# Performance work log

Measured on AMD Instinct MI355X. Metric: run time of the kernel, lower is better.

## Reference

```python
import jax, jax.numpy as jnp
import numpy as np

L = 32            # fixed label space replacing torch.unique (labels in [0, L))
DELTA_AGG = 0.5
DELTA_DIS = 1.5
REG_W = 0.001


def safe_norm(sq):
    # sqrt with zero-safe gradient: returns 0 where sq == 0
    safe = jnp.where(sq > 0, sq, 1.0)
    return jnp.where(sq > 0, jnp.sqrt(safe), 0.0)


def _single(emb, instance, kernel, training_mask):
    D = emb.shape[0]
    tm = training_mask > 0.5
    kn = kernel > 0.5
    inst = jnp.where(tm, instance, 0).reshape(-1)          # (N,) masked instance labels
    inst_k = jnp.where(tm & kn, instance, 0).reshape(-1)   # (N,) kernel-region labels
    embf = emb.reshape(D, -1).T                            # (N, D)
    ones = jnp.ones(inst.shape, dtype=jnp.float32)

    # per-label kernel means (emb_mean), label 0 stays zero as in torch
    cnt_k = jax.ops.segment_sum(ones, inst_k, num_segments=L)            # (L,)
    sum_k = jax.ops.segment_sum(embf, inst_k, num_segments=L)            # (L, D)
    emb_mean = sum_k / jnp.maximum(cnt_k, 1.0)[:, None]
    emb_mean = emb_mean.at[0].set(0.0)

    present = cnt_k > 0
    num_instance = jnp.sum(present.astype(jnp.int32))
    nz = present & (jnp.arange(L) > 0)

    # aggregation loss: per-pixel distance to own instance's kernel mean
    diff = embf - emb_mean[inst]                                          # (N, D)
    dist = safe_norm(jnp.sum(diff * diff, axis=1))
    val = jnp.log(jax.nn.relu(dist - DELTA_AGG) ** 2 + 1.0)
    sum_v = jax.ops.segment_sum(val, inst, num_segments=L)
    cnt = jax.ops.segment_sum(ones, inst, num_segments=L)
    l_agg_per = sum_v / jnp.maximum(cnt, 1.0)
    l_agg = jnp.sum(jnp.where(nz, l_agg_per, 0.0)) / jnp.maximum(num_instance - 1, 1)

    # discrimination loss: all pairs of distinct non-background present labels
    pdiff = emb_mean[:, None, :] - emb_mean[None, :, :]                   # (L, L, D)
    pdist = safe_norm(jnp.sum(pdiff * pdiff, axis=-1))
    pval = jnp.log(jax.nn.relu(2.0 * DELTA_DIS - pdist) ** 2 + 1.0)
    pmask = nz[:, None] & nz[None, :] & ~jnp.eye(L, dtype=bool)
    n_pairs = jnp.sum(pmask.astype(jnp.float32))
    l_dis = jnp.sum(jnp.where(pmask, pval, 0.0)) / jnp.maximum(n_pairs, 1.0)
    l_dis = jnp.where(num_instance > 2, l_dis, 0.0)

    # regularizer over the num_instance present columns of emb_mean
    reg = jnp.log(safe_norm(jnp.sum(emb_mean * emb_mean, axis=1)) + 1.0)
    l_reg = jnp.sum(jnp.where(present, reg, 0.0)) / jnp.maximum(num_instance, 1) * REG_W

    loss = l_agg + l_dis + l_reg
    return jnp.where(num_instance <= 1, 0.0, loss)


def setup_inputs() -> dict:
    key = jax.random.key(0)
    k1, k2, k3, k4 = jax.random.split(key, 4)
    B, D, H, W = 8, 4, 736, 736
    emb = jax.random.normal(k1, (B, D, H, W), dtype=jnp.float32)
    instance = jax.random.randint(k2, (B, H, W), 0, L, dtype=jnp.int32)
    kernel = jax.random.uniform(k3, (B, H, W), dtype=jnp.float32)
    training_mask = jax.random.uniform(k4, (B, H, W), dtype=jnp.float32)
    return {"emb": emb, "instance": instance, "kernel": kernel, "training_mask": training_mask}


def reference(emb, instance, kernel, training_mask):
    return jax.vmap(_single)(emb, instance, kernel, training_mask)
```

## Files before the change

kernel.cpp:

```cpp
#include <hip/hip_runtime.h>

#define LBL 32
#define NPIX (736 * 736)
#define NQ (NPIX / 4)
#define QPB 512
#define NBA 265
#define BATCH 8
#define DELTA_AGG 0.5f
#define DELTA_DIS 1.5f
#define REG_W 0.001f

#define LAB_BASE 0
#define PA_BASE (BATCH * NQ)
#define RED_BASE (PA_BASE + BATCH * NBA * 160)
#define PC_BASE (RED_BASE + BATCH * 256)

__global__ __launch_bounds__(256) void kA(
    const float* __restrict__ emb, const int* __restrict__ inst,
    const float* __restrict__ kern, const float* __restrict__ mask,
    float* __restrict__ ws) {
  const int b = blockIdx.y;
  const int t = threadIdx.x;
  __shared__ float s_cnt[LBL];
  __shared__ float s_sum[LBL * 4];
  if (t < LBL) s_cnt[t] = 0.f;
  if (t < LBL * 4) s_sum[t] = 0.f;
  __syncthreads();

  const long base = (long)b * NPIX;
  const float* eb = emb + (long)b * 4 * NPIX;
  const int4* ip = (const int4*)(inst + base);
  const float4* kp = (const float4*)(kern + base);
  const float4* mp = (const float4*)(mask + base);
  const float4* p0 = (const float4*)(eb);
  const float4* p1 = (const float4*)(eb + NPIX);
  const float4* p2 = (const float4*)(eb + 2 * NPIX);
  const float4* p3 = (const float4*)(eb + 3 * NPIX);

  const int q0 = blockIdx.x * QPB + t;
  const int q1 = q0 + 256;
  const bool v1 = (q1 < NQ);

  const int4 iva = ip[q0];
  const float4 kva = kp[q0], mva = mp[q0];
  const float4 ea0 = p0[q0], ea1 = p1[q0], ea2 = p2[q0], ea3 = p3[q0];
  int4 ivb;
  float4 kvb, mvb, eb0, eb1, eb2, eb3;
  if (v1) {
    ivb = ip[q1]; kvb = kp[q1]; mvb = mp[q1];
    eb0 = p0[q1]; eb1 = p1[q1]; eb2 = p2[q1]; eb3 = p3[q1];
  }

  bool has0 = false;
  unsigned int* labp = (unsigned int*)(ws + LAB_BASE) + (size_t)b * NQ;

  {
    const int labs[4] = {iva.x, iva.y, iva.z, iva.w};
    const float ks[4] = {kva.x, kva.y, kva.z, kva.w};
    const float ms[4] = {mva.x, mva.y, mva.z, mva.w};
    const float c0[4] = {ea0.x, ea0.y, ea0.z, ea0.w};
    const float c1[4] = {ea1.x, ea1.y, ea1.z, ea1.w};
    const float c2[4] = {ea2.x, ea2.y, ea2.z, ea2.w};
    const float c3[4] = {ea3.x, ea3.y, ea3.z, ea3.w};
    unsigned int labw = 0;
#pragma unroll
    for (int j = 0; j < 4; j++) {
      const bool m = ms[j] > 0.5f;
      const int li = m ? labs[j] : 0;
      const int lk = (m && ks[j] > 0.5f) ? labs[j] : 0;
      labw |= ((unsigned int)li) << (8 * j);
      if (lk > 0) {
        atomicAdd(&s_cnt[lk], 1.0f);
        atomicAdd(&s_sum[lk * 4 + 0], c0[j]);
        atomicAdd(&s_sum[lk * 4 + 1], c1[j]);
        atomicAdd(&s_sum[lk * 4 + 2], c2[j]);
        atomicAdd(&s_sum[lk * 4 + 3], c3[j]);
      } else {
        has0 = true;
      }
    }
    labp[q0] = labw;
  }
  if (v1) {
    const int labs[4] = {ivb.x, ivb.y, ivb.z, ivb.w};
    const float ks[4] = {kvb.x, kvb.y, kvb.z, kvb.w};
    const float ms[4] = {mvb.x, mvb.y, mvb.z, mvb.w};
    const float c0[4] = {eb0.x, eb0.y, eb0.z, eb0.w};
    const float c1[4] = {eb1.x, eb1.y, eb1.z, eb1.w};
    const float c2[4] = {eb2.x, eb2.y, eb2.z, eb2.w};
    const float c3[4] = {eb3.x, eb3.y, eb3.z, eb3.w};
    unsigned int labw = 0;
#pragma unroll
    for (int j = 0; j < 4; j++) {
      const bool m = ms[j] > 0.5f;
      const int li = m ? labs[j] : 0;
      const int lk = (m && ks[j] > 0.5f) ? labs[j] : 0;
      labw |= ((unsigned int)li) << (8 * j);
      if (lk > 0) {
        atomicAdd(&s_cnt[lk], 1.0f);
        atomicAdd(&s_sum[lk * 4 + 0], c0[j]);
        atomicAdd(&s_sum[lk * 4 + 1], c1[j]);
        atomicAdd(&s_sum[lk * 4 + 2], c2[j]);
        atomicAdd(&s_sum[lk * 4 + 3], c3[j]);
      } else {
        has0 = true;
      }
    }
    labp[q1] = labw;
  }

  if (has0) s_cnt[0] = 1.0f;
  __syncthreads();
  float* po = ws + PA_BASE + ((size_t)b * NBA + blockIdx.x) * 160;
  if (t < 160) po[t] = (t < 32) ? s_cnt[t] : s_sum[t - 32];
}

__global__ __launch_bounds__(256) void kB(float* __restrict__ ws) {
  const int b = blockIdx.y;
  const int col = blockIdx.x * 4 + (threadIdx.x >> 6);
  const int lane = threadIdx.x & 63;
  const float* pa = ws + PA_BASE + (size_t)b * NBA * 160 + col;
  float s = 0.f;
  for (int g = lane; g < NBA; g += 64) s += pa[(size_t)g * 160];
#pragma unroll
  for (int o = 32; o > 0; o >>= 1) s += __shfl_down(s, o);
  if (lane == 0) ws[RED_BASE + b * 256 + col] = s;
}

__global__ __launch_bounds__(256) void kC(
    const float* __restrict__ emb, float* __restrict__ ws) {
  const int b = blockIdx.y;
  const int t = threadIdx.x;
  __shared__ float s_mean[LBL * 4];
  __shared__ float s_val[LBL];
  __shared__ float s_cta[LBL];
  const float* rd = ws + RED_BASE + b * 256;
  if (t < LBL * 4) {
    const int l = t >> 2;
    s_mean[t] = (l == 0) ? 0.f : rd[32 + t] / fmaxf(rd[l], 1.0f);
  }
  if (t < LBL) {
    s_val[t] = 0.f;
    s_cta[t] = 0.f;
  }
  __syncthreads();

  const float* ebase = emb + (long)b * 4 * NPIX;
  const float4* p0 = (const float4*)(ebase);
  const float4* p1 = (const float4*)(ebase + NPIX);
  const float4* p2 = (const float4*)(ebase + 2 * NPIX);
  const float4* p3 = (const float4*)(ebase + 3 * NPIX);
  const unsigned int* labp = (const unsigned int*)(ws + LAB_BASE) + (size_t)b * NQ;

  const int q0 = blockIdx.x * QPB + t;
  const int q1 = q0 + 256;
  const bool v1 = (q1 < NQ);

  const unsigned int lwa = labp[q0];
  const float4 ea0 = p0[q0], ea1 = p1[q0], ea2 = p2[q0], ea3 = p3[q0];
  unsigned int lwb = 0;
  float4 eb0, eb1, eb2, eb3;
  if (v1) {
    lwb = labp[q1];
    eb0 = p0[q1]; eb1 = p1[q1]; eb2 = p2[q1]; eb3 = p3[q1];
  }

  {
    const float c0[4] = {ea0.x, ea0.y, ea0.z, ea0.w};
    const float c1[4] = {ea1.x, ea1.y, ea1.z, ea1.w};
    const float c2[4] = {ea2.x, ea2.y, ea2.z, ea2.w};
    const float c3[4] = {ea3.x, ea3.y, ea3.z, ea3.w};
#pragma unroll
    for (int j = 0; j < 4; j++) {
      const int li = (lwa >> (8 * j)) & 0xFF;
      if (li > 0) {
        const float d0 = c0[j] - s_mean[li * 4 + 0];
        const float d1 = c1[j] - s_mean[li * 4 + 1];
        const float d2 = c2[j] - s_mean[li * 4 + 2];
        const float d3 = c3[j] - s_mean[li * 4 + 3];
        const float sq = d0 * d0 + d1 * d1 + d2 * d2 + d3 * d3;
        const float dist = (sq > 0.f) ? sqrtf(sq) : 0.f;
        const float tt = fmaxf(dist - DELTA_AGG, 0.f);
        atomicAdd(&s_val[li], logf(fmaf(tt, tt, 1.0f)));
        atomicAdd(&s_cta[li], 1.0f);
      }
    }
  }
  if (v1) {
    const float c0[4] = {eb0.x, eb0.y, eb0.z, eb0.w};
    const float c1[4] = {eb1.x, eb1.y, eb1.z, eb1.w};
    const float c2[4] = {eb2.x, eb2.y, eb2.z, eb2.w};
    const float c3[4] = {eb3.x, eb3.y, eb3.z, eb3.w};
#pragma unroll
    for (int j = 0; j < 4; j++) {
      const int li = (lwb >> (8 * j)) & 0xFF;
      if (li > 0) {
        const float d0 = c0[j] - s_mean[li * 4 + 0];
        const float d1 = c1[j] - s_mean[li * 4 + 1];
        const float d2 = c2[j] - s_mean[li * 4 + 2];
        const float d3 = c3[j] - s_mean[li * 4 + 3];
        const float sq = d0 * d0 + d1 * d1 + d2 * d2 + d3 * d3;
        const float dist = (sq > 0.f) ? sqrtf(sq) : 0.f;
        const float tt = fmaxf(dist - DELTA_AGG, 0.f);
        atomicAdd(&s_val[li], logf(fmaf(tt, tt, 1.0f)));
        atomicAdd(&s_cta[li], 1.0f);
      }
    }
  }
  __syncthreads();
  float* po = ws + PC_BASE + ((size_t)b * NBA + blockIdx.x) * 64;
  if (t < 64) po[t] = (t < 32) ? s_val[t] : s_cta[t - 32];
}

__global__ __launch_bounds__(1024) void kD(const float* __restrict__ ws,
                                           float* __restrict__ out) {
  const int b = blockIdx.x;
  const int t = threadIdx.x;
  const int col = t >> 4, sub = t & 15;
  const float* pc = ws + PC_BASE + (size_t)b * NBA * 64 + col;
  float s = 0.f;
  for (int g = sub; g < NBA; g += 16) s += pc[(size_t)g * 64];
  __shared__ float red[64][17];
  red[col][sub] = s;

  const float* rd = ws + RED_BASE + b * 256;
  __shared__ float sm[LBL * 4];
  __shared__ float scc[LBL];
  if (t >= 512 && t < 640) {
    const int e = t - 512, l = e >> 2;
    sm[e] = (l == 0) ? 0.f : rd[32 + e] / fmaxf(rd[l], 1.0f);
  } else if (t >= 640 && t < 672) {
    scc[t - 640] = rd[t - 640];
  }
  __syncthreads();
  __shared__ float svca[64];
  if (t < 64) {
    float v = 0.f;
#pragma unroll
    for (int k = 0; k < 16; k++) v += red[t][k];
    svca[t] = v;
  }
  __syncthreads();

  if (t < 64) {
    const int lane = t;
    const bool pres = (lane < LBL) && (scc[lane & 31] > 0.f);
    const unsigned long long bal_p = __ballot(pres);
    const int num_instance = __popcll(bal_p);
    const bool nz = pres && (lane > 0);
    const unsigned long long bal_nz = __ballot(nz);

    float agg = 0.f;
    if (nz) agg = svca[lane] / fmaxf(svca[32 + lane], 1.0f);

    float reg = 0.f;
    if (pres) {
      float sq = 0.f;
#pragma unroll
      for (int d = 0; d < 4; d++) sq += sm[lane * 4 + d] * sm[lane * 4 + d];
      const float nrm = (sq > 0.f) ? sqrtf(sq) : 0.f;
      reg = logf(nrm + 1.0f);
    }

    float dis = 0.f, npair = 0.f;
    for (int pi = lane; pi < LBL * LBL; pi += 64) {
      const int i = pi >> 5, j = pi & 31;
      if (i != j && ((bal_nz >> i) & 1ull) && ((bal_nz >> j) & 1ull)) {
        float sq = 0.f;
#pragma unroll
        for (int d = 0; d < 4; d++) {
          const float df = sm[i * 4 + d] - sm[j * 4 + d];
          sq += df * df;
        }
        const float pdist = (sq > 0.f) ? sqrtf(sq) : 0.f;
        const float tt = fmaxf(2.0f * DELTA_DIS - pdist, 0.f);
        dis += logf(fmaf(tt, tt, 1.0f));
        npair += 1.0f;
      }
    }

#pragma unroll
    for (int o = 32; o > 0; o >>= 1) {
      agg += __shfl_down(agg, o);
      reg += __shfl_down(reg, o);
      dis += __shfl_down(dis, o);
      npair += __shfl_down(npair, o);
    }

    if (lane == 0) {
      const float l_agg = agg / fmaxf((float)(num_instance - 1), 1.0f);
      const float l_dis = (num_instance > 2) ? dis / fmaxf(npair, 1.0f) : 0.f;
      const float l_reg = reg / fmaxf((float)num_instance, 1.0f) * REG_W;
      const float loss = l_agg + l_dis + l_reg;
      out[b] = (num_instance <= 1) ? 0.f : loss;
    }
  }
}

extern "C" void kernel_launch(void* const* d_in, const int* in_sizes, int n_in,
                              void* d_out, int out_size, void* d_ws,
                              size_t ws_size, hipStream_t stream) {
  const float* emb = (const float*)d_in[0];
  const int* instance = (const int*)d_in[1];
  const float* kern = (const float*)d_in[2];
  const float* mask = (const float*)d_in[3];
  float* out = (float*)d_out;
  float* ws = (float*)d_ws;

  dim3 gridA(NBA, BATCH);
  kA<<<gridA, 256, 0, stream>>>(emb, instance, kern, mask, ws);
  dim3 gridB(40, BATCH);
  kB<<<gridB, 256, 0, stream>>>(ws);
  kC<<<gridA, 256, 0, stream>>>(emb, ws);
  kD<<<BATCH, 1024, 0, stream>>>(ws, out);
}
```

Baseline: 196.1 us.

## Cache bf16 copy of embeddings in first pass, reuse in aggregation pass

The first pass now writes a packed bf16 copy of the four embedding channels per pixel into the workspace. It also counts the masked instance pixels there, so the aggregation kernel no longer reads the fp32 embeddings or does the count atomics. The aggregation kernel reads 8 bytes per pixel instead of 16, and the partial-sum layouts and the final reduction are adjusted to match. In exchange, the first pass writes extra data, and the per-pixel distances are computed from bf16-rounded embeddings, which reduces accuracy.

```diff
diff --git a/kernel.cpp b/kernel.cpp
--- a/kernel.cpp
+++ b/kernel.cpp
@@ -10,10 +10,23 @@
 #define DELTA_DIS 1.5f
 #define REG_W 0.001f
 
-#define LAB_BASE 0
-#define PA_BASE (BATCH * NQ)
-#define RED_BASE (PA_BASE + BATCH * NBA * 160)
+#define CE_BASE 0
+#define LAB_BASE (BATCH * NPIX * 2)
+#define PA_BASE (LAB_BASE + BATCH * NQ)
+#define RED_BASE (PA_BASE + BATCH * NBA * 192)
 #define PC_BASE (RED_BASE + BATCH * 256)
+
+__device__ __forceinline__ unsigned short f2bf(float f) {
+  unsigned int u = __float_as_uint(f);
+  unsigned int r = u + 0x7FFFu + ((u >> 16) & 1u);
+  return (unsigned short)(r >> 16);
+}
+__device__ __forceinline__ float bfl(unsigned int w) {
+  return __uint_as_float(w << 16);
+}
+__device__ __forceinline__ float bfh(unsigned int w) {
+  return __uint_as_float(w & 0xFFFF0000u);
+}
 
 __global__ __launch_bounds__(256) void kA(
     const float* __restrict__ emb, const int* __restrict__ inst,
@@ -23,19 +36,20 @@
   const int t = threadIdx.x;
   __shared__ float s_cnt[LBL];
   __shared__ float s_sum[LBL * 4];
-  if (t < LBL) s_cnt[t] = 0.f;
+  __shared__ float s_cta[LBL];
+  if (t < LBL) { s_cnt[t] = 0.f; s_cta[t] = 0.f; }
   if (t < LBL * 4) s_sum[t] = 0.f;
   __syncthreads();
 
   const long base = (long)b * NPIX;
-  const float* eb = emb + (long)b * 4 * NPIX;
+  const float* ebase = emb + (long)b * 4 * NPIX;
   const int4* ip = (const int4*)(inst + base);
   const float4* kp = (const float4*)(kern + base);
   const float4* mp = (const float4*)(mask + base);
-  const float4* p0 = (const float4*)(eb);
-  const float4* p1 = (const float4*)(eb + NPIX);
-  const float4* p2 = (const float4*)(eb + 2 * NPIX);
-  const float4* p3 = (const float4*)(eb + 3 * NPIX);
+  const float4* p0 = (const float4*)(ebase);
+  const float4* p1 = (const float4*)(ebase + NPIX);
+  const float4* p2 = (const float4*)(ebase + 2 * NPIX);
+  const float4* p3 = (const float4*)(ebase + 3 * NPIX);
 
   const int q0 = blockIdx.x * QPB + t;
   const int q1 = q0 + 256;
@@ -45,14 +59,15 @@
   const float4 kva = kp[q0], mva = mp[q0];
   const float4 ea0 = p0[q0], ea1 = p1[q0], ea2 = p2[q0], ea3 = p3[q0];
   int4 ivb;
-  float4 kvb, mvb, eb0, eb1, eb2, eb3;
+  float4 kvb, mvb, fb0, fb1, fb2, fb3;
   if (v1) {
     ivb = ip[q1]; kvb = kp[q1]; mvb = mp[q1];
-    eb0 = p0[q1]; eb1 = p1[q1]; eb2 = p2[q1]; eb3 = p3[q1];
+    fb0 = p0[q1]; fb1 = p1[q1]; fb2 = p2[q1]; fb3 = p3[q1];
   }
 
   bool has0 = false;
   unsigned int* labp = (unsigned int*)(ws + LAB_BASE) + (size_t)b * NQ;
+  uint4* cep = (uint4*)(ws + CE_BASE) + (size_t)b * NQ * 2;
 
   {
     const int labs[4] = {iva.x, iva.y, iva.z, iva.w};
@@ -63,12 +78,18 @@
     const float c2[4] = {ea2.x, ea2.y, ea2.z, ea2.w};
     const float c3[4] = {ea3.x, ea3.y, ea3.z, ea3.w};
     unsigned int labw = 0;
+    union { unsigned short us[16]; uint4 v[2]; } pk;
 #pragma unroll
     for (int j = 0; j < 4; j++) {
       const bool m = ms[j] > 0.5f;
       const int li = m ? labs[j] : 0;
       const int lk = (m && ks[j] > 0.5f) ? labs[j] : 0;
       labw |= ((unsigned int)li) << (8 * j);
+      pk.us[j * 4 + 0] = f2bf(c0[j]);
+      pk.us[j * 4 + 1] = f2bf(c1[j]);
+      pk.us[j * 4 + 2] = f2bf(c2[j]);
+      pk.us[j * 4 + 3] = f2bf(c3[j]);
+      if (li > 0) atomicAdd(&s_cta[li], 1.0f);
       if (lk > 0) {
         atomicAdd(&s_cnt[lk], 1.0f);
         atomicAdd(&s_sum[lk * 4 + 0], c0[j]);
@@ -80,22 +101,30 @@
       }
     }
     labp[q0] = labw;
+    cep[(size_t)q0 * 2] = pk.v[0];
+    cep[(size_t)q0 * 2 + 1] = pk.v[1];
   }
   if (v1) {
     const int labs[4] = {ivb.x, ivb.y, ivb.z, ivb.w};
     const float ks[4] = {kvb.x, kvb.y, kvb.z, kvb.w};
     const float ms[4] = {mvb.x, mvb.y, mvb.z, mvb.w};
-    const float c0[4] = {eb0.x, eb0.y, eb0.z, eb0.w};
-    const float c1[4] = {eb1.x, eb1.y, eb1.z, eb1.w};
-    const float c2[4] = {eb2.x, eb2.y, eb2.z, eb2.w};
-    const float c3[4] = {eb3.x, eb3.y, eb3.z, eb3.w};
+    const float c0[4] = {fb0.x, fb0.y, fb0.z, fb0.w};
+    const float c1[4] = {fb1.x, fb1.y, fb1.z, fb1.w};
+    const float c2[4] = {fb2.x, fb2.y, fb2.z, fb2.w};
+    const float c3[4] = {fb3.x, fb3.y, fb3.z, fb3.w};
     unsigned int labw = 0;
+    union { unsigned short us[16]; uint4 v[2]; } pk;
 #pragma unroll
     for (int j = 0; j < 4; j++) {
       const bool m = ms[j] > 0.5f;
       const int li = m ? labs[j] : 0;
       const int lk = (m && ks[j] > 0.5f) ? labs[j] : 0;
       labw |= ((unsigned int)li) << (8 * j);
+      pk.us[j * 4 + 0] = f2bf(c0[j]);
+      pk.us[j * 4 + 1] = f2bf(c1[j]);
+      pk.us[j * 4 + 2] = f2bf(c2[j]);
+      pk.us[j * 4 + 3] = f2bf(c3[j]);
+      if (li > 0) atomicAdd(&s_cta[li], 1.0f);
       if (lk > 0) {
         atomicAdd(&s_cnt[lk], 1.0f);
         atomicAdd(&s_sum[lk * 4 + 0], c0[j]);
@@ -107,138 +136,129 @@
       }
     }
     labp[q1] = labw;
+    cep[(size_t)q1 * 2] = pk.v[0];
+    cep[(size_t)q1 * 2 + 1] = pk.v[1];
   }
 
   if (has0) s_cnt[0] = 1.0f;
   __syncthreads();
-  float* po = ws + PA_BASE + ((size_t)b * NBA + blockIdx.x) * 160;
-  if (t < 160) po[t] = (t < 32) ? s_cnt[t] : s_sum[t - 32];
+  float* po = ws + PA_BASE + ((size_t)b * NBA + blockIdx.x) * 192;
+  if (t < 192)
+    po[t] = (t < 32) ? s_cnt[t] : (t < 160 ? s_sum[t - 32] : s_cta[t - 160]);
 }
 
 __global__ __launch_bounds__(256) void kB(float* __restrict__ ws) {
   const int b = blockIdx.y;
   const int col = blockIdx.x * 4 + (threadIdx.x >> 6);
   const int lane = threadIdx.x & 63;
-  const float* pa = ws + PA_BASE + (size_t)b * NBA * 160 + col;
+  const float* pa = ws + PA_BASE + (size_t)b * NBA * 192 + col;
   float s = 0.f;
-  for (int g = lane; g < NBA; g += 64) s += pa[(size_t)g * 160];
+  for (int g = lane; g < NBA; g += 64) s += pa[(size_t)g * 192];
 #pragma unroll
   for (int o = 32; o > 0; o >>= 1) s += __shfl_down(s, o);
   if (lane == 0) ws[RED_BASE + b * 256 + col] = s;
 }
 
-__global__ __launch_bounds__(256) void kC(
-    const float* __restrict__ emb, float* __restrict__ ws) {
+__global__ __launch_bounds__(256) void kC(float* __restrict__ ws) {
   const int b = blockIdx.y;
   const int t = threadIdx.x;
   __shared__ float s_mean[LBL * 4];
   __shared__ float s_val[LBL];
-  __shared__ float s_cta[LBL];
   const float* rd = ws + RED_BASE + b * 256;
   if (t < LBL * 4) {
     const int l = t >> 2;
     s_mean[t] = (l == 0) ? 0.f : rd[32 + t] / fmaxf(rd[l], 1.0f);
   }
-  if (t < LBL) {
-    s_val[t] = 0.f;
-    s_cta[t] = 0.f;
-  }
-  __syncthreads();
-
-  const float* ebase = emb + (long)b * 4 * NPIX;
-  const float4* p0 = (const float4*)(ebase);
-  const float4* p1 = (const float4*)(ebase + NPIX);
-  const float4* p2 = (const float4*)(ebase + 2 * NPIX);
-  const float4* p3 = (const float4*)(ebase + 3 * NPIX);
+  if (t < LBL) s_val[t] = 0.f;
+  __syncthreads();
+
   const unsigned int* labp = (const unsigned int*)(ws + LAB_BASE) + (size_t)b * NQ;
-
+  const uint4* cep = (const uint4*)(ws + CE_BASE) + (size_t)b * NQ * 2;
   const int q0 = blockIdx.x * QPB + t;
   const int q1 = q0 + 256;
   const bool v1 = (q1 < NQ);
 
   const unsigned int lwa = labp[q0];
-  const float4 ea0 = p0[q0], ea1 = p1[q0], ea2 = p2[q0], ea3 = p3[q0];
+  const uint4 ra0 = cep[(size_t)q0 * 2], ra1 = cep[(size_t)q0 * 2 + 1];
   unsigned int lwb = 0;
-  float4 eb0, eb1, eb2, eb3;
+  uint4 rb0, rb1;
   if (v1) {
     lwb = labp[q1];
-    eb0 = p0[q1]; eb1 = p1[q1]; eb2 = p2[q1]; eb3 = p3[q1];
+    rb0 = cep[(size_t)q1 * 2];
+    rb1 = cep[(size_t)q1 * 2 + 1];
   }
 
   {
-    const float c0[4] = {ea0.x, ea0.y, ea0.z, ea0.w};
-    const float c1[4] = {ea1.x, ea1.y, ea1.z, ea1.w};
-    const float c2[4] = {ea2.x, ea2.y, ea2.z, ea2.w};
-    const float c3[4] = {ea3.x, ea3.y, ea3.z, ea3.w};
+    const unsigned int wlo[4] = {ra0.x, ra0.z, ra1.x, ra1.z};
+    const unsigned int whi[4] = {ra0.y, ra0.w, ra1.y, ra1.w};
 #pragma unroll
     for (int j = 0; j < 4; j++) {
       const int li = (lwa >> (8 * j)) & 0xFF;
       if (li > 0) {
-        const float d0 = c0[j] - s_mean[li * 4 + 0];
-        const float d1 = c1[j] - s_mean[li * 4 + 1];
-        const float d2 = c2[j] - s_mean[li * 4 + 2];
-        const float d3 = c3[j] - s_mean[li * 4 + 3];
+        const float d0 = bfl(wlo[j]) - s_mean[li * 4 + 0];
+        const float d1 = bfh(wlo[j]) - s_mean[li * 4 + 1];
+        const float d2 = bfl(whi[j]) - s_mean[li * 4 + 2];
+        const float d3 = bfh(whi[j]) - s_mean[li * 4 + 3];
         const float sq = d0 * d0 + d1 * d1 + d2 * d2 + d3 * d3;
         const float dist = (sq > 0.f) ? sqrtf(sq) : 0.f;
         const float tt = fmaxf(dist - DELTA_AGG, 0.f);
         atomicAdd(&s_val[li], logf(fmaf(tt, tt, 1.0f)));
-        atomicAdd(&s_cta[li], 1.0f);
       }
     }
   }
   if (v1) {
-    const float c0[4] = {eb0.x, eb0.y, eb0.z, eb0.w};
-    const float c1[4] = {eb1.x, eb1.y, eb1.z, eb1.w};
-    const float c2[4] = {eb2.x, eb2.y, eb2.z, eb2.w};
-    const float c3[4] = {eb3.x, eb3.y, eb3.z, eb3.w};
+    const unsigned int wlo[4] = {rb0.x, rb0.z, rb1.x, rb1.z};
+    const unsigned int whi[4] = {rb0.y, rb0.w, rb1.y, rb1.w};
 #pragma unroll
     for (int j = 0; j < 4; j++) {
       const int li = (lwb >> (8 * j)) & 0xFF;
       if (li > 0) {
-        const float d0 = c0[j] - s_mean[li * 4 + 0];
-        const float d1 = c1[j] - s_mean[li * 4 + 1];
-        const float d2 = c2[j] - s_mean[li * 4 + 2];
-        const float d3 = c3[j] - s_mean[li * 4 + 3];
+        const float d0 = bfl(wlo[j]) - s_mean[li * 4 + 0];
+        const float d1 = bfh(wlo[j]) - s_mean[li * 4 + 1];
+        const float d2 = bfl(whi[j]) - s_mean[li * 4 + 2];
+        const float d3 = bfh(whi[j]) - s_mean[li * 4 + 3];
         const float sq = d0 * d0 + d1 * d1 + d2 * d2 + d3 * d3;
         const float dist = (sq > 0.f) ? sqrtf(sq) : 0.f;
         const float tt = fmaxf(dist - DELTA_AGG, 0.f);
         atomicAdd(&s_val[li], logf(fmaf(tt, tt, 1.0f)));
-        atomicAdd(&s_cta[li], 1.0f);
-      }
-    }
-  }
-  __syncthreads();
-  float* po = ws + PC_BASE + ((size_t)b * NBA + blockIdx.x) * 64;
-  if (t < 64) po[t] = (t < 32) ? s_val[t] : s_cta[t - 32];
+      }
+    }
+  }
+  __syncthreads();
+  float* po = ws + PC_BASE + ((size_t)b * NBA + blockIdx.x) * 32;
+  if (t < 32) po[t] = s_val[t];
 }
 
 __global__ __launch_bounds__(1024) void kD(const float* __restrict__ ws,
                                            float* __restrict__ out) {
   const int b = blockIdx.x;
   const int t = threadIdx.x;
-  const int col = t >> 4, sub = t & 15;
-  const float* pc = ws + PC_BASE + (size_t)b * NBA * 64 + col;
+  const int col = t >> 5, sub = t & 31;
+  const float* pc = ws + PC_BASE + (size_t)b * NBA * 32 + col;
   float s = 0.f;
-  for (int g = sub; g < NBA; g += 16) s += pc[(size_t)g * 64];
-  __shared__ float red[64][17];
+  for (int g = sub; g < NBA; g += 32) s += pc[(size_t)g * 32];
+  __shared__ float red[LBL][33];
   red[col][sub] = s;
 
   const float* rd = ws + RED_BASE + b * 256;
   __shared__ float sm[LBL * 4];
   __shared__ float scc[LBL];
+  __shared__ float sca[LBL];
   if (t >= 512 && t < 640) {
     const int e = t - 512, l = e >> 2;
     sm[e] = (l == 0) ? 0.f : rd[32 + e] / fmaxf(rd[l], 1.0f);
   } else if (t >= 640 && t < 672) {
     scc[t - 640] = rd[t - 640];
-  }
-  __syncthreads();
-  __shared__ float svca[64];
-  if (t < 64) {
+  } else if (t >= 672 && t < 704) {
+    sca[t - 672] = rd[160 + (t - 672)];
+  }
+  __syncthreads();
+  __shared__ float sv[LBL];
+  if (t < 32) {
     float v = 0.f;
 #pragma unroll
-    for (int k = 0; k < 16; k++) v += red[t][k];
-    svca[t] = v;
+    for (int k = 0; k < 32; k++) v += red[t][k];
+    sv[t] = v;
   }
   __syncthreads();
 
@@ -251,7 +271,7 @@
     const unsigned long long bal_nz = __ballot(nz);
 
     float agg = 0.f;
-    if (nz) agg = svca[lane] / fmaxf(svca[32 + lane], 1.0f);
+    if (nz) agg = sv[lane] / fmaxf(sca[lane], 1.0f);
 
     float reg = 0.f;
     if (pres) {
@@ -309,8 +329,8 @@
 
   dim3 gridA(NBA, BATCH);
   kA<<<gridA, 256, 0, stream>>>(emb, instance, kern, mask, ws);
-  dim3 gridB(40, BATCH);
+  dim3 gridB(48, BATCH);
   kB<<<gridB, 256, 0, stream>>>(ws);
-  kC<<<gridA, 256, 0, stream>>>(emb, ws);
+  kC<<<gridA, 256, 0, stream>>>(ws);
   kD<<<BATCH, 1024, 0, stream>>>(ws, out);
 }
```

Result: faster. 182.4 us (-7.0%).
